# Kernel tuning notes

Hardware: AMD Instinct MI355X
Metric: run time of the kernel (lower is better)

## Reference

```python
import jax, jax.numpy as jnp
import numpy as np

NUM_GRAPHS = 512


def setup_inputs() -> dict:
    key = jax.random.key(0)
    ks = jax.random.split(key, 16)
    N, E = 50000, 800000
    x = jax.random.normal(ks[0], (N, 3), dtype=jnp.float32)
    edge_index = jax.random.randint(ks[1], (2, E), 0, N, dtype=jnp.int64)
    batch = jnp.sort(jax.random.randint(ks[2], (N,), 0, NUM_GRAPHS, dtype=jnp.int64))

    def glorot(k, shape):
        fan_in, fan_out = shape
        lim = (6.0 / (fan_in + fan_out)) ** 0.5
        return jax.random.uniform(k, shape, jnp.float32, -lim, lim)

    return {
        "x": x, "edge_index": edge_index, "batch": batch,
        "W1": glorot(ks[3], (3, 32)),   "b1": jnp.zeros((32,), jnp.float32),
        "W2": glorot(ks[4], (32, 64)),  "b2": jnp.zeros((64,), jnp.float32),
        "W3": glorot(ks[5], (64, 128)), "b3": jnp.zeros((128,), jnp.float32),
        "Wf1": glorot(ks[6], (128, 32)), "bf1": jnp.zeros((32,), jnp.float32),
        "Wf2": glorot(ks[7], (32, 4)),   "bf2": jnp.zeros((4,), jnp.float32),
    }


def _gcn_conv(x, src, dst, norm, W, b, N):
    # GCNConv: h = x W, then symmetric-normalized aggregation, then bias.
    h = x @ W                                   # [N, out]
    msg = h[src] * norm[:, None]                # [E+N, out] gathered edge messages
    out = jax.ops.segment_sum(msg, dst, num_segments=N)
    return out + b


def reference(x, edge_index, batch, W1, b1, W2, b2, W3, b3, Wf1, bf1, Wf2, bf2):
    N = x.shape[0]
    loops = jnp.arange(N, dtype=edge_index.dtype)
    src = jnp.concatenate([edge_index[0], loops])   # add self-loops (GCNConv default)
    dst = jnp.concatenate([edge_index[1], loops])
    # symmetric normalization deg^-1/2[src] * deg^-1/2[dst], deg counted on dst
    deg = jax.ops.segment_sum(jnp.ones_like(dst, dtype=x.dtype), dst, num_segments=N)
    dinv = jnp.where(deg > 0, jax.lax.rsqrt(deg), 0.0)
    norm = dinv[src] * dinv[dst]                    # [E+N]

    h = jax.nn.relu(_gcn_conv(x, src, dst, norm, W1, b1, N))
    h = jax.nn.relu(_gcn_conv(h, src, dst, norm, W2, b2, N))
    h = jax.nn.relu(_gcn_conv(h, src, dst, norm, W3, b3, N))

    # global mean pool over graphs
    sums = jax.ops.segment_sum(h, batch, num_segments=NUM_GRAPHS)
    cnts = jax.ops.segment_sum(jnp.ones((N,), h.dtype), batch, num_segments=NUM_GRAPHS)
    pooled = sums / jnp.maximum(cnts, 1.0)[:, None]   # [G, 128]

    z = jax.nn.relu(pooled @ Wf1 + bf1)
    return z @ Wf2 + bf2                              # [G, 4]
```

## Files before the change

### kernel.cpp

```cpp
#include <hip/hip_runtime.h>

#define NN 50000
#define NE 800000
#define NG 512
#define CAP 64
#define NP 196
#define CH 3200
#define NCH 250

__global__ __launch_bounds__(256) void p1_hist_k(const int4* __restrict__ dst4,
                                                 int* __restrict__ Ht,
                                                 int* __restrict__ tot) {
    __shared__ int lh[NP];
    int t = threadIdx.x, b = blockIdx.x;
    if (t < NP) lh[t] = 0;
    __syncthreads();
    int i0 = b * (CH / 4);
    for (int i = i0 + t; i < i0 + CH / 4; i += 256) {
        int4 d = dst4[i];
        atomicAdd(&lh[d.x >> 8], 1);
        atomicAdd(&lh[d.y >> 8], 1);
        atomicAdd(&lh[d.z >> 8], 1);
        atomicAdd(&lh[d.w >> 8], 1);
    }
    __syncthreads();
    if (t < NP) {
        Ht[t * NCH + b] = lh[t];
        atomicAdd(&tot[t], lh[t]);
    }
}

__global__ __launch_bounds__(256) void p2_k(int* __restrict__ Ht,
                                            const int* __restrict__ tot,
                                            int* __restrict__ start) {
    __shared__ int sh[256];
    int p = blockIdx.x, t = threadIdx.x;
    sh[t] = (t < p) ? tot[t] : 0;
    __syncthreads();
    for (int off = 128; off > 0; off >>= 1) {
        if (t < off) sh[t] += sh[t + off];
        __syncthreads();
    }
    int start_p = sh[0];
    __syncthreads();
    if (t == 0) start[p] = start_p;
    if (p == 0 && t == 1) start[NP] = NE;
    int v = (t < NCH) ? Ht[p * NCH + t] : 0;
    sh[t] = v;
    __syncthreads();
    for (int off = 1; off < 256; off <<= 1) {
        int x = (t >= off) ? sh[t - off] : 0;
        __syncthreads();
        sh[t] += x;
        __syncthreads();
    }
    if (t < NCH) Ht[p * NCH + t] = start_p + sh[t] - v;
}

__global__ __launch_bounds__(256) void p3_place_k(const int4* __restrict__ src4,
                                                  const int4* __restrict__ dst4,
                                                  const int* __restrict__ Ht,
                                                  int* __restrict__ pak) {
    __shared__ int cur[NP];
    int t = threadIdx.x, b = blockIdx.x;
    if (t < NP) cur[t] = Ht[t * NCH + b];
    __syncthreads();
    int i0 = b * (CH / 4);
    for (int i = i0 + t; i < i0 + CH / 4; i += 256) {
        int4 d = dst4[i];
        int4 s = src4[i];
        int pos;
        pos = atomicAdd(&cur[d.x >> 8], 1); pak[pos] = s.x | ((d.x & 255) << 16);
        pos = atomicAdd(&cur[d.y >> 8], 1); pak[pos] = s.y | ((d.y & 255) << 16);
        pos = atomicAdd(&cur[d.z >> 8], 1); pak[pos] = s.z | ((d.z & 255) << 16);
        pos = atomicAdd(&cur[d.w >> 8], 1); pak[pos] = s.w | ((d.w & 255) << 16);
    }
}

__global__ __launch_bounds__(256) void p4_build_k(const int* __restrict__ pak,
                                                   const int* __restrict__ start,
                                                   const float* __restrict__ x,
                                                   int* __restrict__ fill,
                                                   float* __restrict__ dinv,
                                                   float* __restrict__ xs,
                                                   int* __restrict__ eidx, int n) {
    __shared__ int lh[256], curn[256];
    int p = blockIdx.x, t = threadIdx.x;
    lh[t] = 0;
    curn[t] = 0;
    __syncthreads();
    int s0 = start[p], s1 = start[p + 1];
    for (int i = s0 + t; i < s1; i += 256) atomicAdd(&lh[pak[i] >> 16], 1);
    __syncthreads();
    int node = p * 256 + t;
    if (node < n) {
        int dg = lh[t];
        fill[node] = dg;
        float d = rsqrtf((float)(dg + 1));
        dinv[node] = d;
        float4 v;
        v.x = x[node * 3 + 0] * d;
        v.y = x[node * 3 + 1] * d;
        v.z = x[node * 3 + 2] * d;
        v.w = 0.0f;
        *(float4*)(xs + (size_t)node * 4) = v;
    }
    __syncthreads();
    for (int i = s0 + t; i < s1; i += 256) {
        int w = pak[i];
        int dl = w >> 16, s = w & 0xFFFF;
        int pos = atomicAdd(&curn[dl], 1) & (CAP - 1);
        eidx[(size_t)(p * 256 + dl) * CAP + pos] = s;
    }
}

__global__ __launch_bounds__(256) void fused_l1_k(
    const int* __restrict__ deg, const int* __restrict__ eidx,
    const float* __restrict__ xs, const float* __restrict__ W1,
    const float* __restrict__ b1, const float* __restrict__ dinv,
    float* __restrict__ A2, int n) {
    __shared__ float act[64][4];
    int t = threadIdx.x;
    int node0 = blockIdx.x * 64;
    {
        int node = node0 + (t >> 2);
        int f = t & 3;
        if (node < n) {
            int e1 = deg[node];
            const int* __restrict__ eb = eidx + node * CAP;
            float acc = xs[(size_t)node * 4 + f];
            int e = 0;
            for (; e + 4 <= e1; e += 4) {
                int4 s = *(const int4*)(eb + e);
                float v0 = xs[(size_t)s.x * 4 + f];
                float v1 = xs[(size_t)s.y * 4 + f];
                float v2 = xs[(size_t)s.z * 4 + f];
                float v3 = xs[(size_t)s.w * 4 + f];
                acc += (v0 + v1) + (v2 + v3);
            }
            for (; e < e1; ++e) acc += xs[(size_t)eb[e] * 4 + f];
            act[t >> 2][f] = acc;
        }
    }
    __syncthreads();
    int f = t & 31;
    int nl0 = t >> 5;
#pragma unroll
    for (int i = 0; i < 8; ++i) {
        int nl = nl0 + i * 8;
        int node = node0 + nl;
        if (node < n) {
            float acc = act[nl][0] * W1[f] + act[nl][1] * W1[32 + f] + act[nl][2] * W1[64 + f];
            float s = dinv[node];
            A2[(size_t)node * 32 + f] = fmaxf(fmaf(s, acc, b1[f]), 0.0f) * s;
        }
    }
}

template <int F>
__global__ __launch_bounds__(256) void gather4_k(const int* __restrict__ deg,
                                                 const int* __restrict__ eidx,
                                                 const float* __restrict__ A,
                                                 float* __restrict__ B, int n) {
    constexpr int FV = F / 4;
    constexpr int NPB = 256 / FV;
    int t = threadIdx.x;
    int node = blockIdx.x * NPB + t / FV;
    int j = (t % FV) * 4;
    if (node >= n) return;
    int e1 = deg[node];
    const int* __restrict__ eb = eidx + node * CAP;
    const float* __restrict__ Aj = A + j;
    float4 a0 = *(const float4*)(Aj + (size_t)node * F);
    float4 a1 = make_float4(0.f, 0.f, 0.f, 0.f);
    float4 a2 = make_float4(0.f, 0.f, 0.f, 0.f);
    float4 a3 = make_float4(0.f, 0.f, 0.f, 0.f);
    int e = 0;
    for (; e + 16 <= e1; e += 16) {
        int4 sa = *(const int4*)(eb + e);
        int4 sb = *(const int4*)(eb + e + 4);
        int4 sc = *(const int4*)(eb + e + 8);
        int4 sd = *(const int4*)(eb + e + 12);
        float4 v0 = *(const float4*)(Aj + (size_t)sa.x * F);
        float4 v1 = *(const float4*)(Aj + (size_t)sa.y * F);
        float4 v2 = *(const float4*)(Aj + (size_t)sa.z * F);
        float4 v3 = *(const float4*)(Aj + (size_t)sa.w * F);
        float4 v4 = *(const float4*)(Aj + (size_t)sb.x * F);
        float4 v5 = *(const float4*)(Aj + (size_t)sb.y * F);
        float4 v6 = *(const float4*)(Aj + (size_t)sb.z * F);
        float4 v7 = *(const float4*)(Aj + (size_t)sb.w * F);
        float4 v8 = *(const float4*)(Aj + (size_t)sc.x * F);
        float4 v9 = *(const float4*)(Aj + (size_t)sc.y * F);
        float4 va = *(const float4*)(Aj + (size_t)sc.z * F);
        float4 vb = *(const float4*)(Aj + (size_t)sc.w * F);
        float4 vc = *(const float4*)(Aj + (size_t)sd.x * F);
        float4 vd = *(const float4*)(Aj + (size_t)sd.y * F);
        float4 ve = *(const float4*)(Aj + (size_t)sd.z * F);
        float4 vf = *(const float4*)(Aj + (size_t)sd.w * F);
        a0.x += (v0.x + v1.x) + (v2.x + v3.x);
        a0.y += (v0.y + v1.y) + (v2.y + v3.y);
        a0.z += (v0.z + v1.z) + (v2.z + v3.z);
        a0.w += (v0.w + v1.w) + (v2.w + v3.w);
        a1.x += (v4.x + v5.x) + (v6.x + v7.x);
        a1.y += (v4.y + v5.y) + (v6.y + v7.y);
        a1.z += (v4.z + v5.z) + (v6.z + v7.z);
        a1.w += (v4.w + v5.w) + (v6.w + v7.w);
        a2.x += (v8.x + v9.x) + (va.x + vb.x);
        a2.y += (v8.y + v9.y) + (va.y + vb.y);
        a2.z += (v8.z + v9.z) + (va.z + vb.z);
        a2.w += (v8.w + v9.w) + (va.w + vb.w);
        a3.x += (vc.x + vd.x) + (ve.x + vf.x);
        a3.y += (vc.y + vd.y) + (ve.y + vf.y);
        a3.z += (vc.z + vd.z) + (ve.z + vf.z);
        a3.w += (vc.w + vd.w) + (ve.w + vf.w);
    }
    for (; e + 4 <= e1; e += 4) {
        int4 sa = *(const int4*)(eb + e);
        float4 v0 = *(const float4*)(Aj + (size_t)sa.x * F);
        float4 v1 = *(const float4*)(Aj + (size_t)sa.y * F);
        float4 v2 = *(const float4*)(Aj + (size_t)sa.z * F);
        float4 v3 = *(const float4*)(Aj + (size_t)sa.w * F);
        a1.x += (v0.x + v1.x) + (v2.x + v3.x);
        a1.y += (v0.y + v1.y) + (v2.y + v3.y);
        a1.z += (v0.z + v1.z) + (v2.z + v3.z);
        a1.w += (v0.w + v1.w) + (v2.w + v3.w);
    }
    for (; e < e1; ++e) {
        float4 v = *(const float4*)(Aj + (size_t)eb[e] * F);
        a0.x += v.x; a0.y += v.y; a0.z += v.z; a0.w += v.w;
    }
    a0.x += (a1.x + a2.x) + a3.x;
    a0.y += (a1.y + a2.y) + a3.y;
    a0.z += (a1.z + a2.z) + a3.z;
    a0.w += (a1.w + a2.w) + a3.w;
    *(float4*)(B + (size_t)node * F + j) = a0;
}

template <int Fin, int Fout, int NPB, bool SCALE_OUT>
__global__ __launch_bounds__(256) void mmB_k(
    const float* __restrict__ G, const float* __restrict__ W,
    const float* __restrict__ bias, const float* __restrict__ dinv,
    float* __restrict__ Aout, int n) {
    constexpr int FL = Fout / 4;
    constexpr int NGRP = 256 / FL;
    constexpr int NPT = NPB / NGRP;
    __shared__ float act[NPB][Fin];
    int t = threadIdx.x;
    int node0 = blockIdx.x * NPB;
    constexpr int TOT4 = NPB * Fin / 4;
    const float4* __restrict__ G4 = (const float4*)(G + (size_t)node0 * Fin);
    float4* act4 = (float4*)&act[0][0];
    for (int i = t; i < TOT4; i += 256) {
        int nl = i / (Fin / 4);
        float4 v = make_float4(0.f, 0.f, 0.f, 0.f);
        if (node0 + nl < n) v = G4[i];
        act4[i] = v;
    }
    __syncthreads();
    int f4 = (t % FL) * 4;
    int nlbase = (t / FL) * NPT;
    float4 acc[NPT];
#pragma unroll
    for (int i = 0; i < NPT; ++i) acc[i] = make_float4(0.f, 0.f, 0.f, 0.f);
    for (int k = 0; k < Fin; k += 4) {
        float4 a[NPT];
#pragma unroll
        for (int i = 0; i < NPT; ++i) a[i] = *(const float4*)&act[nlbase + i][k];
#pragma unroll
        for (int kk = 0; kk < 4; ++kk) {
            float4 w = *(const float4*)(W + (size_t)(k + kk) * Fout + f4);
#pragma unroll
            for (int i = 0; i < NPT; ++i) {
                float av = (&a[i].x)[kk];
                acc[i].x = fmaf(av, w.x, acc[i].x);
                acc[i].y = fmaf(av, w.y, acc[i].y);
                acc[i].z = fmaf(av, w.z, acc[i].z);
                acc[i].w = fmaf(av, w.w, acc[i].w);
            }
        }
    }
    float4 bv = *(const float4*)(bias + f4);
#pragma unroll
    for (int i = 0; i < NPT; ++i) {
        int node = node0 + nlbase + i;
        if (node < n) {
            float s = dinv[node];
            float4 o;
            o.x = fmaxf(fmaf(s, acc[i].x, bv.x), 0.0f);
            o.y = fmaxf(fmaf(s, acc[i].y, bv.y), 0.0f);
            o.z = fmaxf(fmaf(s, acc[i].z, bv.z), 0.0f);
            o.w = fmaxf(fmaf(s, acc[i].w, bv.w), 0.0f);
            if (SCALE_OUT) { o.x *= s; o.y *= s; o.z *= s; o.w *= s; }
            *(float4*)(Aout + (size_t)node * Fout + f4) = o;
        }
    }
}

__device__ __forceinline__ int lbound_d(const int* __restrict__ a, int n, int key) {
    int lo = 0, hi = n;
    while (lo < hi) {
        int m = (lo + hi) >> 1;
        if (a[m] < key) lo = m + 1; else hi = m;
    }
    return lo;
}

__global__ __launch_bounds__(256) void poolhead_k(
    const float* __restrict__ H, const int* __restrict__ batch,
    const float* __restrict__ Wf1, const float* __restrict__ bf1,
    const float* __restrict__ Wf2, const float* __restrict__ bf2,
    float* __restrict__ out, int n) {
    __shared__ int bnd[2];
    __shared__ float pm2[2][128];
    __shared__ float z[32];
    int g = blockIdx.x, t = threadIdx.x;
    if (t == 0) bnd[0] = lbound_d(batch, n, g);
    if (t == 1) bnd[1] = lbound_d(batch, n, g + 1);
    __syncthreads();
    int lo = bnd[0], hi = bnd[1];
    int f = t & 127, r = t >> 7;
    float s0 = 0.f, s1 = 0.f;
    int i = lo + r;
    for (; i + 2 < hi; i += 4) {
        s0 += H[(size_t)i * 128 + f];
        s1 += H[(size_t)(i + 2) * 128 + f];
    }
    if (i < hi) s0 += H[(size_t)i * 128 + f];
    pm2[r][f] = s0 + s1;
    __syncthreads();
    if (t < 128) {
        float c = fmaxf((float)(hi - lo), 1.0f);
        pm2[0][t] = (pm2[0][t] + pm2[1][t]) / c;
    }
    __syncthreads();
    if (t < 32) {
        float acc = bf1[t];
#pragma unroll 4
        for (int k = 0; k < 128; ++k) acc = fmaf(pm2[0][k], Wf1[k * 32 + t], acc);
        z[t] = fmaxf(acc, 0.0f);
    }
    __syncthreads();
    if (t < 4) {
        float acc = bf2[t];
#pragma unroll
        for (int jj = 0; jj < 32; ++jj) acc = fmaf(z[jj], Wf2[jj * 4 + t], acc);
        out[g * 4 + t] = acc;
    }
}

extern "C" void kernel_launch(void* const* d_in, const int* in_sizes, int n_in,
                              void* d_out, int out_size, void* d_ws, size_t ws_size,
                              hipStream_t stream) {
    const float* x    = (const float*)d_in[0];
    const int*   ei   = (const int*)d_in[1];
    const int*   batch= (const int*)d_in[2];
    const float* W1   = (const float*)d_in[3];
    const float* b1   = (const float*)d_in[4];
    const float* W2   = (const float*)d_in[5];
    const float* b2   = (const float*)d_in[6];
    const float* W3   = (const float*)d_in[7];
    const float* b3   = (const float*)d_in[8];
    const float* Wf1  = (const float*)d_in[9];
    const float* bf1  = (const float*)d_in[10];
    const float* Wf2  = (const float*)d_in[11];
    const float* bf2  = (const float*)d_in[12];
    float* out = (float*)d_out;

    int*   fill   = (int*)d_ws;
    float* dinv   = (float*)(fill + NN);
    float* xs     = dinv + NN;
    float* A2     = xs + (size_t)NN * 4;
    float* A3     = A2 + (size_t)NN * 32;
    float* H3     = A3 + (size_t)NN * 64;
    float* G      = H3 + (size_t)NN * 128;
    int*   eidx   = (int*)(G + (size_t)NN * 64);

    int* pak   = (int*)G;
    int* Ht    = (int*)H3;
    int* tot   = Ht + NP * NCH;
    int* start = tot + NP;

    const int4* src4 = (const int4*)ei;
    const int4* dst4 = (const int4*)(ei + NE);

    hipMemsetAsync(tot, 0, NP * 4, stream);
    p1_hist_k<<<NCH, 256, 0, stream>>>(dst4, Ht, tot);
    p2_k<<<NP, 256, 0, stream>>>(Ht, tot, start);
    p3_place_k<<<NCH, 256, 0, stream>>>(src4, dst4, Ht, pak);
    p4_build_k<<<NP, 256, 0, stream>>>(pak, start, x, fill, dinv, xs, eidx, NN);

    fused_l1_k<<<(NN + 63) / 64, 256, 0, stream>>>(fill, eidx, xs, W1, b1, dinv, A2, NN);

    gather4_k<32><<<(NN + 31) / 32, 256, 0, stream>>>(fill, eidx, A2, G, NN);
    mmB_k<32, 64, 32, true><<<(NN + 31) / 32, 256, 0, stream>>>(G, W2, b2, dinv, A3, NN);

    gather4_k<64><<<(NN + 15) / 16, 256, 0, stream>>>(fill, eidx, A3, G, NN);
    mmB_k<64, 128, 32, false><<<(NN + 31) / 32, 256, 0, stream>>>(G, W3, b3, dinv, H3, NN);

    poolhead_k<<<NG, 256, 0, stream>>>(H3, batch, Wf1, bf1, Wf2, bf2, out, NN);
}
```

Baseline: 224.5 us.

## Sort nodes into degree bins to balance gather work across threads

Adds a degree histogram, scan and placement pass that builds a permutation of nodes grouped by in-degree. The layer-1 fused kernel and the gather kernels then process nodes in this order, so threads in a wavefront have similar edge counts and less divergence. The cost is two extra small kernel launches and an extra indirection through perm, with scattered reads of node rows and, in the layer-1 kernel, scattered writes of A2. Degree is clamped to 63 in degp, which is consistent with the existing CAP=64 slot limit.

After: 231.1 us. +2.9%, slower.

```diff
diff --git a/kernel.cpp b/kernel.cpp
--- a/kernel.cpp
+++ b/kernel.cpp
@@ -83,11 +83,13 @@
                                                    int* __restrict__ fill,
                                                    float* __restrict__ dinv,
                                                    float* __restrict__ xs,
-                                                   int* __restrict__ eidx, int n) {
-    __shared__ int lh[256], curn[256];
+                                                   int* __restrict__ eidx,
+                                                   int* __restrict__ bins, int n) {
+    __shared__ int lh[256], curn[256], binh[64];
     int p = blockIdx.x, t = threadIdx.x;
     lh[t] = 0;
     curn[t] = 0;
+    if (t < 64) binh[t] = 0;
     __syncthreads();
     int s0 = start[p], s1 = start[p + 1];
     for (int i = s0 + t; i < s1; i += 256) atomicAdd(&lh[pak[i] >> 16], 1);
@@ -96,6 +98,7 @@
     if (node < n) {
         int dg = lh[t];
         fill[node] = dg;
+        atomicAdd(&binh[min(dg, 63)], 1);
         float d = rsqrtf((float)(dg + 1));
         dinv[node] = d;
         float4 v;
@@ -106,6 +109,7 @@
         *(float4*)(xs + (size_t)node * 4) = v;
     }
     __syncthreads();
+    if (t < 64 && binh[t] > 0) atomicAdd(&bins[t], binh[t]);
     for (int i = s0 + t; i < s1; i += 256) {
         int w = pak[i];
         int dl = w >> 16, s = w & 0xFFFF;
@@ -114,19 +118,65 @@
     }
 }
 
+__global__ __launch_bounds__(64) void p5_binscan_k(const int* __restrict__ bins,
+                                                   int* __restrict__ binstart) {
+    __shared__ int sh[64];
+    int t = threadIdx.x;
+    int v = bins[t];
+    sh[t] = v;
+    __syncthreads();
+    for (int off = 1; off < 64; off <<= 1) {
+        int x = (t >= off) ? sh[t - off] : 0;
+        __syncthreads();
+        sh[t] += x;
+        __syncthreads();
+    }
+    binstart[t] = sh[t] - v;
+}
+
+__global__ __launch_bounds__(256) void p6_binplace_k(const int* __restrict__ fill,
+                                                     const int* __restrict__ binstart,
+                                                     int* __restrict__ bincur,
+                                                     int* __restrict__ perm,
+                                                     int* __restrict__ degp, int n) {
+    __shared__ int binh[64], base[64], cur2[64];
+    int t = threadIdx.x;
+    int node = blockIdx.x * 256 + t;
+    if (t < 64) { binh[t] = 0; cur2[t] = 0; }
+    __syncthreads();
+    int dg = 0;
+    if (node < n) {
+        dg = min(fill[node], 63);
+        atomicAdd(&binh[dg], 1);
+    }
+    __syncthreads();
+    if (t < 64 && binh[t] > 0) base[t] = atomicAdd(&bincur[t], binh[t]);
+    __syncthreads();
+    if (node < n) {
+        int r = atomicAdd(&cur2[dg], 1);
+        int pos = binstart[dg] + base[dg] + r;
+        perm[pos] = node;
+        degp[pos] = dg;
+    }
+}
+
 __global__ __launch_bounds__(256) void fused_l1_k(
-    const int* __restrict__ deg, const int* __restrict__ eidx,
+    const int* __restrict__ degp, const int* __restrict__ perm,
+    const int* __restrict__ eidx,
     const float* __restrict__ xs, const float* __restrict__ W1,
     const float* __restrict__ b1, const float* __restrict__ dinv,
     float* __restrict__ A2, int n) {
     __shared__ float act[64][4];
+    __shared__ int nd[64];
     int t = threadIdx.x;
-    int node0 = blockIdx.x * 64;
+    int i0 = blockIdx.x * 64;
     {
-        int node = node0 + (t >> 2);
+        int i = i0 + (t >> 2);
         int f = t & 3;
-        if (node < n) {
-            int e1 = deg[node];
+        if (i < n) {
+            int node = perm[i];
+            if (f == 0) nd[t >> 2] = node;
+            int e1 = degp[i];
             const int* __restrict__ eb = eidx + node * CAP;
             float acc = xs[(size_t)node * 4 + f];
             int e = 0;
@@ -146,10 +196,11 @@
     int f = t & 31;
     int nl0 = t >> 5;
 #pragma unroll
-    for (int i = 0; i < 8; ++i) {
-        int nl = nl0 + i * 8;
-        int node = node0 + nl;
-        if (node < n) {
+    for (int q = 0; q < 8; ++q) {
+        int nl = nl0 + q * 8;
+        int i = i0 + nl;
+        if (i < n) {
+            int node = nd[nl];
             float acc = act[nl][0] * W1[f] + act[nl][1] * W1[32 + f] + act[nl][2] * W1[64 + f];
             float s = dinv[node];
             A2[(size_t)node * 32 + f] = fmaxf(fmaf(s, acc, b1[f]), 0.0f) * s;
@@ -158,17 +209,19 @@
 }
 
 template <int F>
-__global__ __launch_bounds__(256) void gather4_k(const int* __restrict__ deg,
+__global__ __launch_bounds__(256) void gather4_k(const int* __restrict__ degp,
+                                                 const int* __restrict__ perm,
                                                  const int* __restrict__ eidx,
                                                  const float* __restrict__ A,
                                                  float* __restrict__ B, int n) {
     constexpr int FV = F / 4;
     constexpr int NPB = 256 / FV;
     int t = threadIdx.x;
-    int node = blockIdx.x * NPB + t / FV;
+    int i = blockIdx.x * NPB + t / FV;
     int j = (t % FV) * 4;
-    if (node >= n) return;
-    int e1 = deg[node];
+    if (i >= n) return;
+    int node = perm[i];
+    int e1 = degp[i];
     const int* __restrict__ eb = eidx + node * CAP;
     const float* __restrict__ Aj = A + j;
     float4 a0 = *(const float4*)(Aj + (size_t)node * F);
@@ -373,28 +426,35 @@
     float* A3     = A2 + (size_t)NN * 32;
     float* H3     = A3 + (size_t)NN * 64;
     float* G      = H3 + (size_t)NN * 128;
-    int*   eidx   = (int*)(G + (size_t)NN * 64);
+    int*   perm   = (int*)(G + (size_t)NN * 64);
+    int*   degp   = perm + NN;
+    int*   eidx   = degp + NN;
 
     int* pak   = (int*)G;
     int* Ht    = (int*)H3;
-    int* tot   = Ht + NP * NCH;
-    int* start = tot + NP;
+    int* tot      = Ht + NP * NCH;
+    int* bins     = tot + NP;
+    int* bincur   = bins + 64;
+    int* start    = bincur + 64;
+    int* binstart = start + NP + 1;
 
     const int4* src4 = (const int4*)ei;
     const int4* dst4 = (const int4*)(ei + NE);
 
-    hipMemsetAsync(tot, 0, NP * 4, stream);
+    hipMemsetAsync(tot, 0, (NP + 128) * 4, stream);
     p1_hist_k<<<NCH, 256, 0, stream>>>(dst4, Ht, tot);
     p2_k<<<NP, 256, 0, stream>>>(Ht, tot, start);
     p3_place_k<<<NCH, 256, 0, stream>>>(src4, dst4, Ht, pak);
-    p4_build_k<<<NP, 256, 0, stream>>>(pak, start, x, fill, dinv, xs, eidx, NN);
-
-    fused_l1_k<<<(NN + 63) / 64, 256, 0, stream>>>(fill, eidx, xs, W1, b1, dinv, A2, NN);
-
-    gather4_k<32><<<(NN + 31) / 32, 256, 0, stream>>>(fill, eidx, A2, G, NN);
+    p4_build_k<<<NP, 256, 0, stream>>>(pak, start, x, fill, dinv, xs, eidx, bins, NN);
+    p5_binscan_k<<<1, 64, 0, stream>>>(bins, binstart);
+    p6_binplace_k<<<NP, 256, 0, stream>>>(fill, binstart, bincur, perm, degp, NN);
+
+    fused_l1_k<<<(NN + 63) / 64, 256, 0, stream>>>(degp, perm, eidx, xs, W1, b1, dinv, A2, NN);
+
+    gather4_k<32><<<(NN + 31) / 32, 256, 0, stream>>>(degp, perm, eidx, A2, G, NN);
     mmB_k<32, 64, 32, true><<<(NN + 31) / 32, 256, 0, stream>>>(G, W2, b2, dinv, A3, NN);
 
-    gather4_k<64><<<(NN + 15) / 16, 256, 0, stream>>>(fill, eidx, A3, G, NN);
+    gather4_k<64><<<(NN + 15) / 16, 256, 0, stream>>>(degp, perm, eidx, A3, G, NN);
     mmB_k<64, 128, 32, false><<<(NN + 31) / 32, 256, 0, stream>>>(G, W3, b3, dinv, H3, NN);
 
     poolhead_k<<<NG, 256, 0, stream>>>(H3, batch, Wf1, bf1, Wf2, bf2, out, NN);
```
